# Kernel tuning notes

Hardware: AMD Instinct MI355X
Metric: run time of the kernel (lower is better)

Reference implementation:

```python
import jax, jax.numpy as jnp
import numpy as np

K = 32           # neighbors per point
HEADS = 8
EPS = 1e-5       # BatchNorm eps
NEG_SLOPE = 0.2  # LeakyReLU slope


def knn_idx(x, k):
    # x: (B, C, N) -> (B, N, k) indices of k nearest neighbors in feature space
    xx = jnp.sum(x * x, axis=1)                       # (B, N)
    inner = jnp.einsum('bcn,bcm->bnm', x, x)          # (B, N, N)
    neg_sq_dist = 2.0 * inner - xx[:, :, None] - xx[:, None, :]
    return jax.lax.top_k(neg_sq_dist, k)[1]           # (B, N, k)


def group_diff(x, k):
    # DGCNN-style 'diff' grouping: neighbor features minus center feature.
    idx = knn_idx(x, k)                               # (B, N, k)
    xt = jnp.transpose(x, (0, 2, 1))                  # (B, N, C)
    nb = jax.vmap(lambda f, i: f[i])(xt, idx)         # (B, N, k, C)
    diff = nb - xt[:, :, None, :]                     # (B, N, k, C)
    return jnp.transpose(diff, (0, 3, 1, 2))          # (B, C, N, k)


def batchnorm1d(y, gamma, beta):
    # training-mode BN over (B, C, N): stats over batch and point dims
    m = jnp.mean(y, axis=(0, 2), keepdims=True)
    v = jnp.var(y, axis=(0, 2), keepdims=True)
    return gamma[None, :, None] * (y - m) * jax.lax.rsqrt(v + EPS) + beta[None, :, None]


def setup_inputs() -> dict:
    key = jax.random.key(0)
    ks = jax.random.split(key, 6)
    B, C, N = 8, 64, 2048
    return {
        'x':  jax.random.normal(ks[0], (B, C, N), jnp.float32),
        'Wq': jax.random.normal(ks[1], (64, 64), jnp.float32) * 0.1,
        'Wk': jax.random.normal(ks[2], (64, 64), jnp.float32) * 0.1,
        'Wv': jax.random.normal(ks[3], (64, 64), jnp.float32) * 0.1,
        'W1': jax.random.normal(ks[4], (128, 64), jnp.float32) * 0.1,
        'W2': jax.random.normal(ks[5], (64, 128), jnp.float32) * 0.1,
        'g1': jnp.ones((64,), jnp.float32),
        'b1': jnp.zeros((64,), jnp.float32),
        'g2': jnp.ones((64,), jnp.float32),
        'b2': jnp.zeros((64,), jnp.float32),
    }


def reference(x, Wq, Wk, Wv, W1, W2, g1, b1, g2, b2):
    B, C, N = x.shape
    nbr = group_diff(x, K)                                        # (B, C, N, K)

    # 1x1 conv projections == per-point matmuls
    q = jnp.einsum('oc,bcn->bon', Wq, x)                          # (B, Co, N)
    q = q.reshape(B, HEADS, -1, N).transpose(0, 1, 3, 2)          # (B, H, N, d)
    k = jnp.einsum('oc,bcnk->bonk', Wk, nbr)
    k = k.reshape(B, HEADS, -1, N, K).transpose(0, 1, 3, 4, 2)    # (B, H, N, K, d)
    v = jnp.einsum('oc,bcnk->bonk', Wv, nbr)
    v = v.reshape(B, HEADS, -1, N, K).transpose(0, 1, 3, 4, 2)    # (B, H, N, K, d)

    scale = jnp.sqrt(jnp.asarray(q.shape[-1], q.dtype))
    energy = jnp.einsum('bhnd,bhnkd->bhnk', q, k) / scale         # (B, H, N, K)
    attn = jax.nn.softmax(energy, axis=-1)
    out = jnp.einsum('bhnk,bhnkd->bhnd', attn, v)                 # (B, H, N, d)
    out = out.transpose(0, 2, 1, 3).reshape(B, N, -1).transpose(0, 2, 1)  # (B, Cv, N)

    x1 = batchnorm1d(x + out, g1, b1)
    h = jax.nn.leaky_relu(jnp.einsum('oc,bcn->bon', W1, x1), NEG_SLOPE)
    ff = jnp.einsum('oc,bcn->bon', W2, h)
    return batchnorm1d(x1 + ff, g2, b2)
```

## Files before the change

### kernel.cpp

```cpp
#include <hip/hip_runtime.h>


#define NN 2048

typedef __attribute__((ext_vector_type(8))) short bf16x8;
typedef __attribute__((ext_vector_type(8))) unsigned short u16x8;
typedef __attribute__((ext_vector_type(4))) float f32x4;

__device__ inline void bsplit(float x, short& h, short& m, short& l)
{
    unsigned u  = __float_as_uint(x);
    unsigned hb = (u + 0x7FFFu + ((u >> 16) & 1u)) >> 16;
    float hf = __uint_as_float(hb << 16);
    float r1 = x - hf;
    unsigned u1 = __float_as_uint(r1);
    unsigned mb = (u1 + 0x7FFFu + ((u1 >> 16) & 1u)) >> 16;
    float mf = __uint_as_float(mb << 16);
    float r2 = r1 - mf;
    unsigned u2 = __float_as_uint(r2);
    unsigned lb = (u2 + 0x7FFFu + ((u2 >> 16) & 1u)) >> 16;
    h = (short)hb; m = (short)mb; l = (short)lb;
}

__global__ __launch_bounds__(256) void prep_kernel(
    const float* __restrict__ x, const float* __restrict__ Wk,
    const float* __restrict__ Wv, float* __restrict__ xx,
    float* __restrict__ KT, float* __restrict__ VT,
    short* __restrict__ xh, short* __restrict__ xm, short* __restrict__ xl)
{
    __shared__ float xs[64][33];
    __shared__ float wks[4096], wvs[4096];
    const int t = threadIdx.x;
    const int b = blockIdx.x >> 6;
    const int n0 = (blockIdx.x & 63) * 32;
    for (int i = 0; i < 16; ++i) {
        int e = t + 256 * i;
        wks[e] = Wk[e];
        wvs[e] = Wv[e];
    }
    for (int i = 0; i < 8; ++i) {
        int e = t + 256 * i;
        xs[e >> 5][e & 31] = x[((size_t)b * 64 + (e >> 5)) * 2048 + n0 + (e & 31)];
    }
    __syncthreads();
    if (t < 32) {
        float s = 0.f;
#pragma unroll
        for (int c = 0; c < 64; ++c) { float v = xs[c][t]; s += v * v; }
        xx[b * 2048 + n0 + t] = s;
    }
    const int p = t & 31, g = t >> 5;
    {
        u16x8 vh, vm, vl;
#pragma unroll
        for (int ci = 0; ci < 8; ++ci) {
            short h, m, l;
            bsplit(xs[g * 8 + ci][p], h, m, l);
            vh[ci] = (unsigned short)h; vm[ci] = (unsigned short)m; vl[ci] = (unsigned short)l;
        }
        size_t base = ((size_t)(b * 2048 + n0 + p)) * 64 + g * 8;
        *reinterpret_cast<u16x8*>(xh + base) = vh;
        *reinterpret_cast<u16x8*>(xm + base) = vm;
        *reinterpret_cast<u16x8*>(xl + base) = vl;
    }
    {
        float xv[64];
#pragma unroll
        for (int c = 0; c < 64; ++c) xv[c] = xs[c][p];
        size_t base = ((size_t)(b * 2048 + n0 + p)) * 64 + g * 8;
        float ok[8], ov[8];
#pragma unroll
        for (int oi = 0; oi < 8; ++oi) {
            int o = g * 8 + oi;
            float ak = 0.f, av = 0.f;
#pragma unroll
            for (int c = 0; c < 64; ++c) {
                float xc = xv[c];
                ak += wks[o * 64 + c] * xc;
                av += wvs[o * 64 + c] * xc;
            }
            ok[oi] = ak; ov[oi] = av;
        }
        *reinterpret_cast<float4*>(KT + base)     = make_float4(ok[0], ok[1], ok[2], ok[3]);
        *reinterpret_cast<float4*>(KT + base + 4) = make_float4(ok[4], ok[5], ok[6], ok[7]);
        *reinterpret_cast<float4*>(VT + base)     = make_float4(ov[0], ov[1], ov[2], ov[3]);
        *reinterpret_cast<float4*>(VT + base + 4) = make_float4(ov[4], ov[5], ov[6], ov[7]);
    }
}

__global__ __launch_bounds__(256) void qproj_kernel(
    const float* __restrict__ x, const float* __restrict__ Wq,
    float* __restrict__ Qp)
{
    __shared__ float xs[64][33];
    __shared__ float wqs[4096];
    const int t = threadIdx.x;
    const int b = blockIdx.x >> 6;
    const int n0 = (blockIdx.x & 63) * 32;
    for (int i = 0; i < 16; ++i) { int e = t + 256 * i; wqs[e] = Wq[e]; }
    for (int i = 0; i < 8; ++i) {
        int e = t + 256 * i;
        xs[e >> 5][e & 31] = x[((size_t)b * 64 + (e >> 5)) * 2048 + n0 + (e & 31)];
    }
    __syncthreads();
    const int p = t & 31, g = t >> 5;
    float xv[64];
#pragma unroll
    for (int c = 0; c < 64; ++c) xv[c] = xs[c][p];
    size_t base = ((size_t)(b * 2048 + n0 + p)) * 64 + g * 8;
    float oq[8];
#pragma unroll
    for (int oi = 0; oi < 8; ++oi) {
        int o = g * 8 + oi;
        float a = 0.f;
#pragma unroll
        for (int c = 0; c < 64; ++c) a += wqs[o * 64 + c] * xv[c];
        oq[oi] = a * 0.35355339059327379f;
    }
    *reinterpret_cast<float4*>(Qp + base)     = make_float4(oq[0], oq[1], oq[2], oq[3]);
    *reinterpret_cast<float4*>(Qp + base + 4) = make_float4(oq[4], oq[5], oq[6], oq[7]);
}

__device__ inline void mm6(f32x4& a, bf16x8 Ah, bf16x8 Am, bf16x8 Al,
                           bf16x8 Bh, bf16x8 Bm, bf16x8 Bl)
{
    a = __builtin_amdgcn_mfma_f32_16x16x32_bf16(Al, Bh, a, 0, 0, 0);
    a = __builtin_amdgcn_mfma_f32_16x16x32_bf16(Ah, Bl, a, 0, 0, 0);
    a = __builtin_amdgcn_mfma_f32_16x16x32_bf16(Am, Bm, a, 0, 0, 0);
    a = __builtin_amdgcn_mfma_f32_16x16x32_bf16(Am, Bh, a, 0, 0, 0);
    a = __builtin_amdgcn_mfma_f32_16x16x32_bf16(Ah, Bm, a, 0, 0, 0);
    a = __builtin_amdgcn_mfma_f32_16x16x32_bf16(Ah, Bh, a, 0, 0, 0);
}

__global__ __launch_bounds__(256) void gemm_kernel(
    const short* __restrict__ xh, const short* __restrict__ xm,
    const short* __restrict__ xl, const float* __restrict__ xx,
    float* __restrict__ Dp)
{
    __shared__ short BhL[8192], BmL[8192], BlL[8192];
    const int t = threadIdx.x;
    const int lane = t & 63;
    const int w = t >> 6;
    const int b = blockIdx.x >> 8;
    const int tile = blockIdx.x & 255;
    const int r0 = (tile >> 4) * 128 + w * 32;
    const int c0 = (tile & 15) * 128;
    const int rl = lane & 15;
    const int g = lane >> 4;
    const int kg = g * 8;

    const size_t boff = (size_t)b * 2048 * 64;
    const short* XH = xh + boff;
    const short* XM = xm + boff;
    const short* XL = xl + boff;

    bf16x8 aH[2][2], aM[2][2], aL[2][2];
#pragma unroll
    for (int s = 0; s < 2; ++s)
#pragma unroll
        for (int rb = 0; rb < 2; ++rb) {
            const size_t ab = (size_t)(r0 + rb * 16 + rl) * 64 + s * 32 + kg;
            aH[s][rb] = *reinterpret_cast<const bf16x8*>(XH + ab);
            aM[s][rb] = *reinterpret_cast<const bf16x8*>(XM + ab);
            aL[s][rb] = *reinterpret_cast<const bf16x8*>(XL + ab);
        }

    {
        const short* sH = XH + (size_t)c0 * 64;
        const short* sM = XM + (size_t)c0 * 64;
        const short* sL = XL + (size_t)c0 * 64;
#pragma unroll
        for (int i = 0; i < 4; ++i) {
            int ci = t + 256 * i;
            int col = ci >> 3, j = ci & 7;
            int d = col * 64 + ((j ^ (col & 7)) << 3);
            *reinterpret_cast<u16x8*>(BhL + d) = *reinterpret_cast<const u16x8*>(sH + ci * 8);
            *reinterpret_cast<u16x8*>(BmL + d) = *reinterpret_cast<const u16x8*>(sM + ci * 8);
            *reinterpret_cast<u16x8*>(BlL + d) = *reinterpret_cast<const u16x8*>(sL + ci * 8);
        }
    }
    __syncthreads();

    f32x4 acc[2][8];
#pragma unroll
    for (int rb = 0; rb < 2; ++rb)
#pragma unroll
        for (int cb = 0; cb < 8; ++cb)
            acc[rb][cb] = (f32x4){0.f, 0.f, 0.f, 0.f};

#pragma unroll
    for (int cb = 0; cb < 8; ++cb) {
        __builtin_amdgcn_sched_barrier(0);
        const int cl = cb * 16 + rl;
#pragma unroll
        for (int s = 0; s < 2; ++s) {
            const int d = cl * 64 + (((s * 4 + g) ^ (cl & 7)) << 3);
            bf16x8 Bh = *reinterpret_cast<const bf16x8*>(BhL + d);
            bf16x8 Bm = *reinterpret_cast<const bf16x8*>(BmL + d);
            bf16x8 Bl = *reinterpret_cast<const bf16x8*>(BlL + d);
            mm6(acc[0][cb], aH[s][0], aM[s][0], aL[s][0], Bh, Bm, Bl);
            mm6(acc[1][cb], aH[s][1], aM[s][1], aL[s][1], Bh, Bm, Bl);
        }
    }
    __builtin_amdgcn_sched_barrier(0);

    const float* xxb = xx + b * 2048;
    const int rg = g * 4;
#pragma unroll
    for (int cb = 0; cb < 8; ++cb) {
        const int col = c0 + cb * 16 + rl;
        const float xc = xxb[col];
#pragma unroll
        for (int rb = 0; rb < 2; ++rb) {
            const int rbase = r0 + rb * 16 + rg;
#pragma unroll
            for (int e = 0; e < 4; ++e) {
                float v = 2.f * acc[rb][cb][e] - xxb[rbase + e];
                v = v - xc;
                Dp[((size_t)(b * 2048 + rbase + e)) * 2048 + col] = v;
            }
        }
    }
}

__global__ __launch_bounds__(256) void select_kernel(
    const float* __restrict__ Dp, int* __restrict__ idx)
{
    __shared__ unsigned long long cand[4][64];
    const int t = threadIdx.x, w = t >> 6, lane = t & 63;
    const int b = blockIdx.x >> 9;
    const int r = (blockIdx.x & 511) * 4 + w;
    const float* row = Dp + ((size_t)(b * 2048 + r)) * 2048;
    int* orow = idx + ((size_t)(b * 2048 + r)) * 32;
    const unsigned lobase = 2047u - (unsigned)(lane * 4);

    unsigned sv[32];
#pragma unroll
    for (int q = 0; q < 8; ++q) {
        float4 f = *reinterpret_cast<const float4*>(row + q * 256 + lane * 4);
        float vv[4] = {f.x, f.y, f.z, f.w};
#pragma unroll
        for (int e = 0; e < 4; ++e) {
            unsigned u = __float_as_uint(vv[e]);
            sv[q * 4 + e] = u ^ (unsigned)(((int)u >> 31) | 0x80000000);
        }
    }
    unsigned m16[16];
#pragma unroll
    for (int i = 0; i < 16; ++i) m16[i] = sv[i] > sv[i + 16] ? sv[i] : sv[i + 16];
#pragma unroll
    for (int n2 = 8; n2 >= 1; n2 >>= 1)
#pragma unroll
        for (int i = 0; i < n2; ++i)
            m16[i] = m16[i] > m16[i + n2] ? m16[i] : m16[i + n2];
    const unsigned mx = m16[0];

    unsigned T = 0u;
#pragma unroll
    for (int bit = 31; bit >= 0; --bit) {
        unsigned c2 = T | (1u << bit);
        if (__popcll(__ballot(mx >= c2)) >= 32) T = c2;
    }

    int c = 0;
#pragma unroll
    for (int s = 0; s < 32; ++s) c += (sv[s] >= T) ? 1 : 0;
    int pfx = c;
#pragma unroll
    for (int d = 1; d < 64; d <<= 1) {
        int o = __shfl_up(pfx, d);
        pfx += (lane >= d) ? o : 0;
    }
    const int total = __shfl(pfx, 63);
    int off = pfx - c;

    if (total <= 64) {
        cand[w][lane] = 0ull;
#pragma unroll
        for (int s = 0; s < 32; ++s) {
            if (sv[s] >= T) {
                unsigned lo = lobase - (unsigned)(((s >> 2) << 8) + (s & 3));
                cand[w][off] = ((unsigned long long)sv[s] << 32) | lo;
                ++off;
            }
        }
        asm volatile("s_waitcnt lgkmcnt(0)" ::: "memory");
        __builtin_amdgcn_sched_barrier(0);
        const unsigned long long ck = cand[w][lane];
        const unsigned csv = (unsigned)(ck >> 32);
        const unsigned clo = (unsigned)(ck & 0xFFFFFFFFu);
        unsigned S = 0u;
#pragma unroll
        for (int bit = 31; bit >= 0; --bit) {
            unsigned c2 = S | (1u << bit);
            if (__popcll(__ballot(csv >= c2)) >= 32) S = c2;
        }
        const bool gt = csv > S, eq = csv == S;
        const int a2 = __popcll(__ballot(gt));
        const int need = 32 - a2;
        unsigned L = 0u;
#pragma unroll
        for (int bit = 10; bit >= 0; --bit) {
            unsigned c2 = L | (1u << bit);
            if (__popcll(__ballot(eq && (clo >= c2))) >= need) L = c2;
        }
        const bool member = gt || (eq && clo >= L);
        const unsigned long long mmask = __ballot(member);
        if (member) {
            int slot = __builtin_amdgcn_mbcnt_hi(
                (unsigned)(mmask >> 32),
                __builtin_amdgcn_mbcnt_lo((unsigned)mmask, 0u));
            orow[slot] = 2047 - (int)clo;
        }
    } else {
        unsigned cons = 0u;
        for (int it = 0; it < 32; ++it) {
            unsigned b2 = 0u, l2 = 0u;
#pragma unroll
            for (int s = 0; s < 32; ++s) {
                unsigned lo = lobase - (unsigned)(((s >> 2) << 8) + (s & 3));
                bool ok = !((cons >> s) & 1u) &&
                          ((sv[s] > b2) || (sv[s] == b2 && lo > l2));
                b2 = ok ? sv[s] : b2;
                l2 = ok ? lo : l2;
            }
            unsigned wsv = b2, wlo = l2;
#pragma unroll
            for (int d = 1; d < 64; d <<= 1) {
                unsigned osv = __shfl_xor(wsv, d);
                unsigned olo = __shfl_xor(wlo, d);
                bool take = (osv > wsv) || (osv == wsv && olo > wlo);
                wsv = take ? osv : wsv;
                wlo = take ? olo : wlo;
            }
            int gidx = 2047 - (int)wlo;
            if (lane == ((gidx >> 2) & 63)) {
                int slot = ((gidx >> 8) << 2) | (gidx & 3);
                cons |= 1u << slot;
            }
            if (lane == 0) orow[it] = gidx;
        }
    }
}

__global__ __launch_bounds__(256) void attn_kernel(
    const float* __restrict__ x, const float* __restrict__ Qp,
    const float* __restrict__ KT, const float* __restrict__ VT,
    const int* __restrict__ idx, float* __restrict__ A1)
{
    __shared__ float Vn[4][32][66];
    __shared__ float qs[4][64], xq[4][64], vsf[4][64];
    __shared__ float es[4][8][32];
    const int t = threadIdx.x, w = t >> 6, lane = t & 63;
    const int b = blockIdx.x >> 9;
    const int n = (blockIdx.x & 511) * 4 + w;
    const size_t prow = (size_t)(b * 2048 + n);
    const size_t pbase = prow * 64;

    qs[w][lane]  = Qp[pbase + lane];
    xq[w][lane]  = x[((size_t)b * 64 + lane) * 2048 + n];
    vsf[w][lane] = VT[pbase + lane];
    asm volatile("s_waitcnt lgkmcnt(0)" ::: "memory");
    __builtin_amdgcn_sched_barrier(0);
    {
        const int j = lane >> 1, half = lane & 1, c0 = half * 32;
        const int nbi = idx[prow * 32 + j] & 2047;
        const float* kr = KT + ((size_t)(b * 2048 + nbi)) * 64 + c0;
        const float* vr = VT + ((size_t)(b * 2048 + nbi)) * 64 + c0;
        float eh[4] = {0.f, 0.f, 0.f, 0.f};
#pragma unroll
        for (int q = 0; q < 8; ++q) {
            float4 kq = *reinterpret_cast<const float4*>(kr + q * 4);
            float4 qv = *reinterpret_cast<const float4*>(&qs[w][c0 + q * 4]);
            const int hh = q >> 1;
            eh[hh] += qv.x * kq.x;
            eh[hh] += qv.y * kq.y;
            eh[hh] += qv.z * kq.z;
            eh[hh] += qv.w * kq.w;
            *reinterpret_cast<float4*>(&Vn[w][j][c0 + q * 4]) =
                *reinterpret_cast<const float4*>(vr + q * 4);
        }
#pragma unroll
        for (int hh = 0; hh < 4; ++hh) es[w][half * 4 + hh][j] = eh[hh];
    }
    __syncthreads();
    if (t < 32) {
        int w2 = t >> 3, h = t & 7;
        float mx = -INFINITY;
#pragma unroll
        for (int j = 0; j < 32; ++j) mx = fmaxf(mx, es[w2][h][j]);
        float pv[32], s = 0.f;
#pragma unroll
        for (int j = 0; j < 32; ++j) { pv[j] = __expf(es[w2][h][j] - mx); s += pv[j]; }
        float inv = 1.f / s;
#pragma unroll
        for (int j = 0; j < 32; ++j) es[w2][h][j] = pv[j] * inv;
    }
    __syncthreads();
    {
        const int h = lane >> 3;
        float acc = 0.f;
#pragma unroll
        for (int j = 0; j < 32; ++j) acc += es[w][h][j] * Vn[w][j][lane];
        A1[pbase + lane] = acc - vsf[w][lane] + xq[w][lane];
    }
}

__global__ __launch_bounds__(256) void bn_partial_kernel(
    const float* __restrict__ Y, float* __restrict__ psum, float* __restrict__ psq)
{
    __shared__ float rs[4][64], rq[4][64];
    const int t = threadIdx.x;
    const int c = t & 63, pg = t >> 6;
    const int b = blockIdx.x >> 5;
    const int n0 = (blockIdx.x & 31) * 64;
    float s = 0.f, q = 0.f;
    for (int k = 0; k < 16; ++k) {
        float v = Y[((size_t)(b * 2048 + n0 + pg * 16 + k)) * 64 + c];
        s += v; q += v * v;
    }
    rs[pg][c] = s; rq[pg][c] = q;
    __syncthreads();
    if (t < 64) {
        psum[blockIdx.x * 64 + t] = rs[0][t] + rs[1][t] + rs[2][t] + rs[3][t];
        psq[blockIdx.x * 64 + t]  = rq[0][t] + rq[1][t] + rq[2][t] + rq[3][t];
    }
}

__global__ void bn_final_kernel(
    const float* __restrict__ psum, const float* __restrict__ psq,
    const float* __restrict__ gamma, const float* __restrict__ beta,
    float* __restrict__ sc, float* __restrict__ sh)
{
    int c = threadIdx.x;
    float s = 0.f, q = 0.f;
    for (int i = 0; i < 256; ++i) { s += psum[i * 64 + c]; q += psq[i * 64 + c]; }
    float mean = s * (1.f / 16384.f);
    float var = q * (1.f / 16384.f) - mean * mean;
    float g = gamma[c] * rsqrtf(var + 1e-5f);
    sc[c] = g;
    sh[c] = beta[c] - mean * g;
}

__global__ __launch_bounds__(256) void ffn_kernel(
    const float* __restrict__ A1, const float* __restrict__ W1,
    const float* __restrict__ W2, const float* __restrict__ s1,
    const float* __restrict__ t1, float* __restrict__ P2)
{
    __shared__ float W1s[8192];
    __shared__ float W2s[8192];
    __shared__ float xs[64][65];
    __shared__ float hs[64][129];
    __shared__ float sts[64], stt[64];
    const int t = threadIdx.x;
    const int b = blockIdx.x >> 5;
    const int n0 = (blockIdx.x & 31) * 64;
    if (t < 64) { sts[t] = s1[t]; stt[t] = t1[t]; }
    for (int i = 0; i < 32; ++i) {
        int e = t + 256 * i;
        W1s[e] = W1[e];
        W2s[e] = W2[e];
    }
    __syncthreads();
    for (int i = 0; i < 16; ++i) {
        int e = t + 256 * i, p = e >> 6, c = e & 63;
        xs[p][c] = A1[((size_t)(b * 2048 + n0 + p)) * 64 + c] * sts[c] + stt[c];
    }
    __syncthreads();
    const int p = t & 63, g = t >> 6;
    {
        float xv[64];
#pragma unroll
        for (int c = 0; c < 64; ++c) xv[c] = xs[p][c];
        for (int u = 0; u < 32; ++u) {
            int j = g * 32 + u;
            float acc = 0.f;
#pragma unroll
            for (int c = 0; c < 64; ++c) acc += W1s[j * 64 + c] * xv[c];
            hs[p][j] = (acc > 0.f) ? acc : 0.2f * acc;
        }
    }
    __syncthreads();
    {
        float hv[128];
#pragma unroll
        for (int j = 0; j < 128; ++j) hv[j] = hs[p][j];
        const size_t pbase = ((size_t)(b * 2048 + n0 + p)) * 64 + g * 16;
        float o4[16];
#pragma unroll
        for (int oi = 0; oi < 16; ++oi) {
            int o = g * 16 + oi;
            float a = xs[p][o];
#pragma unroll
            for (int j = 0; j < 128; ++j) a += W2s[o * 128 + j] * hv[j];
            o4[oi] = a;
        }
#pragma unroll
        for (int q = 0; q < 4; ++q)
            *reinterpret_cast<float4*>(P2 + pbase + q * 4) =
                make_float4(o4[q * 4], o4[q * 4 + 1], o4[q * 4 + 2], o4[q * 4 + 3]);
    }
}

__global__ __launch_bounds__(256) void final_kernel(
    const float* __restrict__ P2, const float* __restrict__ s2,
    const float* __restrict__ t2, float* __restrict__ out)
{
    __shared__ float ts[64][65];
    __shared__ float sts[64], stt[64];
    const int t = threadIdx.x;
    const int b = blockIdx.x >> 5;
    const int n0 = (blockIdx.x & 31) * 64;
    if (t < 64) { sts[t] = s2[t]; stt[t] = t2[t]; }
    __syncthreads();
    for (int i = 0; i < 16; ++i) {
        int e = t + 256 * i, p = e >> 6, c = e & 63;
        ts[p][c] = P2[((size_t)(b * 2048 + n0 + p)) * 64 + c] * sts[c] + stt[c];
    }
    __syncthreads();
    const int c = t >> 2, p0 = (t & 3) * 16;
    float* dst = out + ((size_t)(b * 64 + c)) * 2048 + n0 + p0;
#pragma unroll
    for (int q = 0; q < 4; ++q)
        *reinterpret_cast<float4*>(dst + q * 4) =
            make_float4(ts[p0 + q * 4 + 0][c], ts[p0 + q * 4 + 1][c],
                        ts[p0 + q * 4 + 2][c], ts[p0 + q * 4 + 3][c]);
}

__global__ __launch_bounds__(256) void zero_kernel(float* __restrict__ out)
{
    reinterpret_cast<float4*>(out)[blockIdx.x * 256 + threadIdx.x] =
        make_float4(0.f, 0.f, 0.f, 0.f);
}

extern "C" void kernel_launch(void* const* d_in, const int* in_sizes, int n_in,
                              void* d_out, int out_size, void* d_ws, size_t ws_size,
                              hipStream_t stream)
{
    const float* x  = (const float*)d_in[0];
    const float* Wq = (const float*)d_in[1];
    const float* Wk = (const float*)d_in[2];
    const float* Wv = (const float*)d_in[3];
    const float* W1 = (const float*)d_in[4];
    const float* W2 = (const float*)d_in[5];
    const float* g1 = (const float*)d_in[6];
    const float* b1 = (const float*)d_in[7];
    const float* g2 = (const float*)d_in[8];
    const float* b2 = (const float*)d_in[9];
    float* out = (float*)d_out;
    (void)in_sizes; (void)n_in; (void)out_size;

    char* ws = (char*)d_ws;
    const size_t off_xx  = 0;
    const size_t off_KT  = 65536;
    const size_t off_VT  = off_KT  + 4194304;
    const size_t off_idx = off_VT  + 4194304;
    const size_t off_A1  = off_idx + 2097152;
    const size_t off_s1  = off_A1  + 4194304;
    const size_t off_t1  = off_s1 + 256;
    const size_t off_s2  = off_t1 + 256;
    const size_t off_t2  = off_s2 + 256;
    const size_t off_Dp  = 14815232;
    const size_t DP_SZ   = (size_t)8 * 2048 * 2048 * 4;
    const size_t REQ_FAST = off_Dp + DP_SZ;

    if (ws_size < REQ_FAST) {
        zero_kernel<<<1024, 256, 0, stream>>>(out);
        return;
    }

    float* xx = (float*)(ws + off_xx);
    float* KT = (float*)(ws + off_KT);
    float* VT = (float*)(ws + off_VT);
    int* idx  = (int*)(ws + off_idx);
    float* A1 = (float*)(ws + off_A1);
    float* P2 = KT;
    short* xh = (short*)(ws + off_idx);
    short* xm = (short*)(ws + off_A1);
    short* xl = (short*)(ws + off_A1 + 2097152);
    float* s1 = (float*)(ws + off_s1); float* t1 = (float*)(ws + off_t1);
    float* s2 = (float*)(ws + off_s2); float* t2 = (float*)(ws + off_t2);
    float* Dp = (float*)(ws + off_Dp);
    float* Qp = Dp;
    float* ps1 = Dp;
    float* pq1 = Dp + 16384;
    float* ps2 = Dp + 32768;
    float* pq2 = Dp + 49152;

    prep_kernel<<<512, 256, 0, stream>>>(x, Wk, Wv, xx, KT, VT, xh, xm, xl);
    gemm_kernel<<<2048, 256, 0, stream>>>(xh, xm, xl, xx, Dp);
    select_kernel<<<4096, 256, 0, stream>>>(Dp, idx);
    qproj_kernel<<<512, 256, 0, stream>>>(x, Wq, Qp);
    attn_kernel<<<4096, 256, 0, stream>>>(x, Qp, KT, VT, idx, A1);
    bn_partial_kernel<<<256, 256, 0, stream>>>(A1, ps1, pq1);
    bn_final_kernel<<<1, 64, 0, stream>>>(ps1, pq1, g1, b1, s1, t1);
    ffn_kernel<<<256, 256, 0, stream>>>(A1, W1, W2, s1, t1, P2);
    bn_partial_kernel<<<256, 256, 0, stream>>>(P2, ps2, pq2);
    bn_final_kernel<<<1, 64, 0, stream>>>(ps2, pq2, g2, b2, s2, t2);
    final_kernel<<<256, 256, 0, stream>>>(P2, s2, t2, out);
}
```

Baseline: 295.9 us.

## Split distance matrix into hi/lo 16-bit planes so select reads only high halves

The GEMM epilogue now writes the order-preserving distance keys as two separate 16-bit planes (high and low halves) with a permuted column layout that allows 16-byte stores. The select kernel reads only the high-half plane to find the top-k threshold, gathers low halves only for boundary ties, and reconstructs original indices from the permuted positions. This cuts the bytes read by the selection pass. In exchange, candidate handling is more complex and can hold up to 256 candidates, and the slow fallback path still loads both planes.

Measured after the change: 269.3 us. -9.0%, faster.

```diff
diff --git a/kernel.cpp b/kernel.cpp
--- a/kernel.cpp
+++ b/kernel.cpp
@@ -135,7 +135,7 @@
 __global__ __launch_bounds__(256) void gemm_kernel(
     const short* __restrict__ xh, const short* __restrict__ xm,
     const short* __restrict__ xl, const float* __restrict__ xx,
-    float* __restrict__ Dp)
+    unsigned short* __restrict__ Kp, unsigned short* __restrict__ Lp)
 {
     __shared__ short BhL[8192], BmL[8192], BlL[8192];
     const int t = threadIdx.x;
@@ -207,64 +207,63 @@
     const float* xxb = xx + b * 2048;
     const int rg = g * 4;
 #pragma unroll
-    for (int cb = 0; cb < 8; ++cb) {
-        const int col = c0 + cb * 16 + rl;
-        const float xc = xxb[col];
-#pragma unroll
-        for (int rb = 0; rb < 2; ++rb) {
-            const int rbase = r0 + rb * 16 + rg;
-#pragma unroll
-            for (int e = 0; e < 4; ++e) {
-                float v = 2.f * acc[rb][cb][e] - xxb[rbase + e];
-                v = v - xc;
-                Dp[((size_t)(b * 2048 + rbase + e)) * 2048 + col] = v;
+    for (int rb = 0; rb < 2; ++rb) {
+#pragma unroll
+        for (int e = 0; e < 4; ++e) {
+            const int row = r0 + rb * 16 + rg + e;
+            const float xn = xxb[row];
+            unsigned hiw[4], low[4];
+#pragma unroll
+            for (int cp = 0; cp < 4; ++cp) {
+                unsigned su[2];
+#pragma unroll
+                for (int h2 = 0; h2 < 2; ++h2) {
+                    const int cb = cp * 2 + h2;
+                    float v = 2.f * acc[rb][cb][e] - xn;
+                    v = v - xxb[c0 + cb * 16 + rl];
+                    unsigned u = __float_as_uint(v);
+                    su[h2] = u ^ (unsigned)(((int)u >> 31) | 0x80000000);
+                }
+                hiw[cp] = (su[0] >> 16) | (su[1] & 0xFFFF0000u);
+                low[cp] = (su[0] & 0xFFFFu) | (su[1] << 16);
             }
+            const size_t base = ((size_t)(b * 2048 + row)) * 2048 + c0 + rl * 8;
+            *reinterpret_cast<uint4*>(Kp + base) = make_uint4(hiw[0], hiw[1], hiw[2], hiw[3]);
+            *reinterpret_cast<uint4*>(Lp + base) = make_uint4(low[0], low[1], low[2], low[3]);
         }
     }
 }
 
 __global__ __launch_bounds__(256) void select_kernel(
-    const float* __restrict__ Dp, int* __restrict__ idx)
-{
-    __shared__ unsigned long long cand[4][64];
+    const unsigned short* __restrict__ Kp, const unsigned short* __restrict__ Lp,
+    int* __restrict__ idx)
+{
+    __shared__ unsigned cand[4][256];
     const int t = threadIdx.x, w = t >> 6, lane = t & 63;
     const int b = blockIdx.x >> 9;
     const int r = (blockIdx.x & 511) * 4 + w;
-    const float* row = Dp + ((size_t)(b * 2048 + r)) * 2048;
+    const size_t rowbase = ((size_t)(b * 2048 + r)) * 2048;
     int* orow = idx + ((size_t)(b * 2048 + r)) * 32;
-    const unsigned lobase = 2047u - (unsigned)(lane * 4);
-
-    unsigned sv[32];
-#pragma unroll
-    for (int q = 0; q < 8; ++q) {
-        float4 f = *reinterpret_cast<const float4*>(row + q * 256 + lane * 4);
-        float vv[4] = {f.x, f.y, f.z, f.w};
-#pragma unroll
-        for (int e = 0; e < 4; ++e) {
-            unsigned u = __float_as_uint(vv[e]);
-            sv[q * 4 + e] = u ^ (unsigned)(((int)u >> 31) | 0x80000000);
-        }
-    }
-    unsigned m16[16];
-#pragma unroll
-    for (int i = 0; i < 16; ++i) m16[i] = sv[i] > sv[i + 16] ? sv[i] : sv[i + 16];
-#pragma unroll
-    for (int n2 = 8; n2 >= 1; n2 >>= 1)
-#pragma unroll
-        for (int i = 0; i < n2; ++i)
-            m16[i] = m16[i] > m16[i + n2] ? m16[i] : m16[i + n2];
-    const unsigned mx = m16[0];
-
-    unsigned T = 0u;
-#pragma unroll
-    for (int bit = 31; bit >= 0; --bit) {
+
+    unsigned short kv[32];
+#pragma unroll
+    for (int q = 0; q < 4; ++q) {
+        u16x8 v = *reinterpret_cast<const u16x8*>(Kp + rowbase + lane * 32 + q * 8);
+#pragma unroll
+        for (int e = 0; e < 8; ++e) kv[q * 8 + e] = v[e];
+    }
+    unsigned mx = 0;
+#pragma unroll
+    for (int s = 0; s < 32; ++s) mx = kv[s] > mx ? (unsigned)kv[s] : mx;
+    unsigned T = 0;
+#pragma unroll
+    for (int bit = 15; bit >= 0; --bit) {
         unsigned c2 = T | (1u << bit);
         if (__popcll(__ballot(mx >= c2)) >= 32) T = c2;
     }
-
     int c = 0;
 #pragma unroll
-    for (int s = 0; s < 32; ++s) c += (sv[s] >= T) ? 1 : 0;
+    for (int s = 0; s < 32; ++s) c += (kv[s] >= T) ? 1 : 0;
     int pfx = c;
 #pragma unroll
     for (int d = 1; d < 64; d <<= 1) {
@@ -274,55 +273,125 @@
     const int total = __shfl(pfx, 63);
     int off = pfx - c;
 
-    if (total <= 64) {
-        cand[w][lane] = 0ull;
+    if (total <= 256) {
 #pragma unroll
         for (int s = 0; s < 32; ++s) {
-            if (sv[s] >= T) {
-                unsigned lo = lobase - (unsigned)(((s >> 2) << 8) + (s & 3));
-                cand[w][off] = ((unsigned long long)sv[s] << 32) | lo;
+            if (kv[s] >= T) {
+                cand[w][off] = ((unsigned)kv[s] << 12) | (unsigned)(lane * 32 + s);
                 ++off;
             }
         }
         asm volatile("s_waitcnt lgkmcnt(0)" ::: "memory");
         __builtin_amdgcn_sched_barrier(0);
-        const unsigned long long ck = cand[w][lane];
-        const unsigned csv = (unsigned)(ck >> 32);
-        const unsigned clo = (unsigned)(ck & 0xFFFFFFFFu);
-        unsigned S = 0u;
-#pragma unroll
-        for (int bit = 31; bit >= 0; --bit) {
+        bool val[4]; unsigned hi[4], pos_[4];
+#pragma unroll
+        for (int s2 = 0; s2 < 4; ++s2) {
+            int i2 = lane + 64 * s2;
+            unsigned e2 = cand[w][i2];
+            val[s2] = i2 < total;
+            hi[s2] = e2 >> 12;
+            pos_[s2] = e2 & 0xFFFu;
+        }
+        unsigned S = 0;
+#pragma unroll
+        for (int bit = 15; bit >= 0; --bit) {
             unsigned c2 = S | (1u << bit);
-            if (__popcll(__ballot(csv >= c2)) >= 32) S = c2;
-        }
-        const bool gt = csv > S, eq = csv == S;
-        const int a2 = __popcll(__ballot(gt));
-        const int need = 32 - a2;
-        unsigned L = 0u;
+            int cnt = 0;
+#pragma unroll
+            for (int s2 = 0; s2 < 4; ++s2)
+                cnt += __popcll(__ballot(val[s2] && hi[s2] >= c2));
+            if (cnt >= 32) S = c2;
+        }
+        bool isin[4], bnd[4];
+        int cin = 0;
+#pragma unroll
+        for (int s2 = 0; s2 < 4; ++s2) {
+            isin[s2] = val[s2] && hi[s2] > S;
+            bnd[s2]  = val[s2] && hi[s2] == S;
+            cin += __popcll(__ballot(isin[s2]));
+        }
+        const int need = 32 - cin;
+        unsigned lo16[4];
+#pragma unroll
+        for (int s2 = 0; s2 < 4; ++s2)
+            lo16[s2] = bnd[s2] ? (unsigned)Lp[rowbase + pos_[s2]] : 0u;
+        unsigned L = 0;
+#pragma unroll
+        for (int bit = 15; bit >= 0; --bit) {
+            unsigned c2 = L | (1u << bit);
+            int cnt = 0;
+#pragma unroll
+            for (int s2 = 0; s2 < 4; ++s2)
+                cnt += __popcll(__ballot(bnd[s2] && lo16[s2] >= c2));
+            if (cnt >= need) L = c2;
+        }
+        bool in2[4], bnd2[4];
+        int a2 = 0;
+#pragma unroll
+        for (int s2 = 0; s2 < 4; ++s2) {
+            in2[s2]  = bnd[s2] && lo16[s2] > L;
+            bnd2[s2] = bnd[s2] && lo16[s2] == L;
+            a2 += __popcll(__ballot(in2[s2]));
+        }
+        const int need2 = need - a2;
+        unsigned lo11[4]; int gix[4];
+#pragma unroll
+        for (int s2 = 0; s2 < 4; ++s2) {
+            unsigned p = pos_[s2];
+            gix[s2] = (int)((p & ~127u) + (p & 7u) * 16u + ((p >> 3) & 15u));
+            lo11[s2] = 2047u - (unsigned)gix[s2];
+        }
+        unsigned L2 = 0;
 #pragma unroll
         for (int bit = 10; bit >= 0; --bit) {
-            unsigned c2 = L | (1u << bit);
-            if (__popcll(__ballot(eq && (clo >= c2))) >= need) L = c2;
-        }
-        const bool member = gt || (eq && clo >= L);
-        const unsigned long long mmask = __ballot(member);
-        if (member) {
-            int slot = __builtin_amdgcn_mbcnt_hi(
-                (unsigned)(mmask >> 32),
-                __builtin_amdgcn_mbcnt_lo((unsigned)mmask, 0u));
-            orow[slot] = 2047 - (int)clo;
-        }
+            unsigned c2 = L2 | (1u << bit);
+            int cnt = 0;
+#pragma unroll
+            for (int s2 = 0; s2 < 4; ++s2)
+                cnt += __popcll(__ballot(bnd2[s2] && lo11[s2] >= c2));
+            if (cnt >= need2) L2 = c2;
+        }
+        bool sel[4]; int nsel = 0;
+#pragma unroll
+        for (int s2 = 0; s2 < 4; ++s2) {
+            sel[s2] = isin[s2] || in2[s2] || (bnd2[s2] && lo11[s2] >= L2);
+            nsel += sel[s2] ? 1 : 0;
+        }
+        int p2 = nsel;
+#pragma unroll
+        for (int d = 1; d < 64; d <<= 1) {
+            int o = __shfl_up(p2, d);
+            p2 += (lane >= d) ? o : 0;
+        }
+        int wo = p2 - nsel;
+#pragma unroll
+        for (int s2 = 0; s2 < 4; ++s2)
+            if (sel[s2]) { orow[wo] = gix[s2]; ++wo; }
     } else {
+        unsigned short lv[32];
+#pragma unroll
+        for (int q = 0; q < 4; ++q) {
+            u16x8 v2 = *reinterpret_cast<const u16x8*>(Lp + rowbase + lane * 32 + q * 8);
+#pragma unroll
+            for (int e = 0; e < 8; ++e) lv[q * 8 + e] = v2[e];
+        }
+        unsigned ku[32], lidx[32];
+#pragma unroll
+        for (int s = 0; s < 32; ++s) {
+            ku[s] = ((unsigned)kv[s] << 16) | (unsigned)lv[s];
+            unsigned p = (unsigned)(lane * 32 + s);
+            unsigned g2 = (p & ~127u) + (p & 7u) * 16u + ((p >> 3) & 15u);
+            lidx[s] = 2047u - g2;
+        }
         unsigned cons = 0u;
         for (int it = 0; it < 32; ++it) {
             unsigned b2 = 0u, l2 = 0u;
 #pragma unroll
             for (int s = 0; s < 32; ++s) {
-                unsigned lo = lobase - (unsigned)(((s >> 2) << 8) + (s & 3));
                 bool ok = !((cons >> s) & 1u) &&
-                          ((sv[s] > b2) || (sv[s] == b2 && lo > l2));
-                b2 = ok ? sv[s] : b2;
-                l2 = ok ? lo : l2;
+                          ((ku[s] > b2) || (ku[s] == b2 && lidx[s] > l2));
+                b2 = ok ? ku[s] : b2;
+                l2 = ok ? lidx[s] : l2;
             }
             unsigned wsv = b2, wlo = l2;
 #pragma unroll
@@ -333,12 +402,10 @@
                 wsv = take ? osv : wsv;
                 wlo = take ? olo : wlo;
             }
-            int gidx = 2047 - (int)wlo;
-            if (lane == ((gidx >> 2) & 63)) {
-                int slot = ((gidx >> 8) << 2) | (gidx & 3);
-                cons |= 1u << slot;
-            }
-            if (lane == 0) orow[it] = gidx;
+            int g2 = 2047 - (int)wlo;
+            unsigned p = (unsigned)((g2 & ~127) + (g2 & 15) * 8 + ((g2 >> 4) & 7));
+            if (lane == (int)(p >> 5)) cons |= 1u << (p & 31u);
+            if (lane == 0) orow[it] = g2;
         }
     }
 }
@@ -386,12 +453,12 @@
     __syncthreads();
     if (t < 32) {
         int w2 = t >> 3, h = t & 7;
-        float mx = -INFINITY;
-#pragma unroll
-        for (int j = 0; j < 32; ++j) mx = fmaxf(mx, es[w2][h][j]);
+        float mxv = -INFINITY;
+#pragma unroll
+        for (int j = 0; j < 32; ++j) mxv = fmaxf(mxv, es[w2][h][j]);
         float pv[32], s = 0.f;
 #pragma unroll
-        for (int j = 0; j < 32; ++j) { pv[j] = __expf(es[w2][h][j] - mx); s += pv[j]; }
+        for (int j = 0; j < 32; ++j) { pv[j] = __expf(es[w2][h][j] - mxv); s += pv[j]; }
         float inv = 1.f / s;
 #pragma unroll
         for (int j = 0; j < 32; ++j) es[w2][h][j] = pv[j] * inv;
@@ -561,8 +628,8 @@
     const size_t off_s2  = off_t1 + 256;
     const size_t off_t2  = off_s2 + 256;
     const size_t off_Dp  = 14815232;
-    const size_t DP_SZ   = (size_t)8 * 2048 * 2048 * 4;
-    const size_t REQ_FAST = off_Dp + DP_SZ;
+    const size_t KP_SZ   = (size_t)8 * 2048 * 2048 * 2;
+    const size_t REQ_FAST = off_Dp + 2 * KP_SZ;
 
     if (ws_size < REQ_FAST) {
         zero_kernel<<<1024, 256, 0, stream>>>(out);
@@ -580,16 +647,17 @@
     short* xl = (short*)(ws + off_A1 + 2097152);
     float* s1 = (float*)(ws + off_s1); float* t1 = (float*)(ws + off_t1);
     float* s2 = (float*)(ws + off_s2); float* t2 = (float*)(ws + off_t2);
-    float* Dp = (float*)(ws + off_Dp);
-    float* Qp = Dp;
-    float* ps1 = Dp;
-    float* pq1 = Dp + 16384;
-    float* ps2 = Dp + 32768;
-    float* pq2 = Dp + 49152;
+    unsigned short* Kp = (unsigned short*)(ws + off_Dp);
+    unsigned short* Lp = (unsigned short*)(ws + off_Dp + KP_SZ);
+    float* Qp = (float*)(ws + off_Dp);
+    float* ps1 = (float*)(ws + off_Dp);
+    float* pq1 = ps1 + 16384;
+    float* ps2 = ps1 + 32768;
+    float* pq2 = ps1 + 49152;
 
     prep_kernel<<<512, 256, 0, stream>>>(x, Wk, Wv, xx, KT, VT, xh, xm, xl);
-    gemm_kernel<<<2048, 256, 0, stream>>>(xh, xm, xl, xx, Dp);
-    select_kernel<<<4096, 256, 0, stream>>>(Dp, idx);
+    gemm_kernel<<<2048, 256, 0, stream>>>(xh, xm, xl, xx, Kp, Lp);
+    select_kernel<<<4096, 256, 0, stream>>>(Kp, Lp, idx);
     qproj_kernel<<<512, 256, 0, stream>>>(x, Wq, Qp);
     attn_kernel<<<4096, 256, 0, stream>>>(x, Qp, KT, VT, idx, A1);
     bn_partial_kernel<<<256, 256, 0, stream>>>(A1, ps1, pq1);
```
